# Optimization experiments

Measured on AMD Instinct MI355X. Metric: run time of the kernel, lower is better.

## Reference

```python
import jax, jax.numpy as jnp
import numpy as np

N, F_IN, F_OUT = 8192, 512, 256


def setup_inputs() -> dict:
    key = jax.random.key(0)
    k1, k2, k3, k4 = jax.random.split(key, 4)
    x = jax.random.normal(k1, (N, F_IN), dtype=jnp.float32)
    adj = jax.random.randint(k2, (N, N), 0, 2, dtype=jnp.int32)
    # xavier-uniform-like init scale for W and a
    wb = 1.414 * np.sqrt(6.0 / (F_IN + F_OUT))
    ab = 1.414 * np.sqrt(6.0 / (2 * F_OUT + 1))
    W = jax.random.uniform(k3, (F_IN, F_OUT), minval=-wb, maxval=wb, dtype=jnp.float32)
    a = jax.random.uniform(k4, (2 * F_OUT, 1), minval=-ab, maxval=ab, dtype=jnp.float32)
    return {"x": x, "adj": adj, "W": W, "a": a, "heads": 4}


def reference(x, adj, W, a, heads):
    # Wh = x @ W : [N, F_OUT]
    Wh = x @ W
    f_out = W.shape[1]
    # a = [a_src; a_dst], so e_ij = leakyrelu(Wh_i . a_src + Wh_j . a_dst)
    s_src = Wh @ a[:f_out, 0]   # [N]
    s_dst = Wh @ a[f_out:, 0]   # [N]
    e = jax.nn.leaky_relu(s_src[:, None] + s_dst[None, :], negative_slope=0.2)  # [N, N]
    # scatter into dense matrix: non-edges hold 0 and DO participate in softmax
    att = jnp.where(adj != 0, e, jnp.zeros((), dtype=e.dtype))
    att = jax.nn.softmax(att, axis=1)
    # dropout is identity in eval mode (self.training=False)
    h = att @ Wh                                  # [N, F_OUT]
    n = x.shape[0]
    h = h.reshape(n, heads, f_out // heads).mean(axis=1)  # multi-head mean
    return h
```

## Files before the change

### kernel.cpp

```cpp
#include <hip/hip_runtime.h>
#include <hip/hip_bf16.h>

#define NN 8192
#define FIN 512
#define FOUT 256
#define FH 64
#define JSPLIT 32
#define JCHUNK (NN / JSPLIT)
#define STEPS (JCHUNK / 32)

typedef float f32x16 __attribute__((ext_vector_type(16)));
typedef short bf16x8 __attribute__((ext_vector_type(8)));
typedef unsigned short us8 __attribute__((ext_vector_type(8)));
typedef unsigned int uint32x4 __attribute__((ext_vector_type(4)));

static __device__ __forceinline__ unsigned short f2bf(float x) {
  unsigned int u = __builtin_bit_cast(unsigned int, x);
  unsigned int r = (u + 0x7fffu + ((u >> 16) & 1u)) >> 16;
  return (unsigned short)r;
}
static __device__ __forceinline__ float bf2f(unsigned short u) {
  unsigned int v = ((unsigned int)u) << 16;
  return __builtin_bit_cast(float, v);
}
static __device__ __forceinline__ float fastexp2(float x) {
  float r;
  asm("v_exp_f32 %0, %1" : "=v"(r) : "v"(x));
  return r;
}
static __device__ __forceinline__ unsigned int pkbf(float a, float b) {
  unsigned int w;
  asm("v_cvt_pk_bf16_f32 %0, %1, %2" : "=v"(w) : "v"(a), "v"(b));
  return w;
}
static __device__ __forceinline__ float lo16f(unsigned int w) {
  return __builtin_bit_cast(float, w << 16);
}
static __device__ __forceinline__ float hi16f(unsigned int w) {
  return __builtin_bit_cast(float, w & 0xffff0000u);
}

__global__ __launch_bounds__(256) void prep_small(const float* __restrict__ W,
                                                  const float* __restrict__ a,
                                                  unsigned short* __restrict__ Bw) {
  const int kt = blockIdx.x;
  __shared__ float wm[16][64];
  __shared__ float wt[16][2];
  const int t = threadIdx.x;
#pragma unroll
  for (int i = 0; i < 4; ++i) {
    const int idx = t + i * 256;
    const int kr = idx >> 6, c = idx & 63;
    const float* wr = W + (size_t)(kt * 16 + kr) * FOUT + c;
    wm[kr][c] = 0.25f * (wr[0] + wr[64] + wr[128] + wr[192]);
  }
  if (t < 32) {
    const int kr = t & 15, sel = t >> 4;
    const float* wr = W + (size_t)(kt * 16 + kr) * FOUT;
    const float* av = a + sel * FOUT;
    float s = 0.f;
    for (int n = 0; n < FOUT; ++n) s += wr[n] * av[n];
    wt[kr][sel] = s * 1.44269504f;
  }
  __syncthreads();
#pragma unroll
  for (int i = 0; i < 12; ++i) {
    const int idx = t + i * 256;
    const int e = idx & 7, n = (idx >> 3) & 31, r2 = idx >> 8;
    const int khb = r2 & 1, q = r2 >> 1;
    const int nf = q % 3, h = q / 3;
    const int k = khb * 8 + e;
    float v = nf < 2 ? wm[k][nf * 32 + n]
                     : (n == 0 ? wt[k][0] : (n == 1 ? wt[k][1] : 0.f));
    const unsigned short hi = f2bf(v);
    Bw[(size_t)kt * 3072 + idx] = (h == 0) ? hi : f2bf(v - bf2f(hi));
  }
}

__global__ __launch_bounds__(192) void gemm_whm(const float* __restrict__ X,
                                                const unsigned short* __restrict__ Bw,
                                                unsigned short* __restrict__ Bg,
                                                float* __restrict__ ssrc,
                                                float* __restrict__ sdst) {
  __shared__ float xs[32][516];
  __shared__ float sred[32][2];
  const int mw = blockIdx.x;
  const int tid = threadIdx.x;
  const float* xb = X + (size_t)(mw * 32) * FIN;
  for (int i = tid; i < 4096; i += 192) {
    const int row = i >> 7, c4 = (i & 127) << 2;
    *(float4*)&xs[row][c4] = *(const float4*)(xb + (size_t)row * FIN + c4);
  }
  __syncthreads();

  const int nf = tid >> 6, lane = tid & 63;
  const int l31 = lane & 31, kh = lane >> 5;
  f32x16 acc = (f32x16)(0.f);
  const unsigned short* bp = Bw + ((size_t)nf * 2 + kh) * 256 + l31 * 8;
#pragma unroll 4
  for (int kt = 0; kt < 32; ++kt) {
    const float* xr = &xs[l31][kt * 16 + kh * 8];
    const float4 va = *(const float4*)xr;
    const float4 vb = *(const float4*)(xr + 4);
    const unsigned int h0 = pkbf(va.x, va.y), h1 = pkbf(va.z, va.w);
    const unsigned int h2 = pkbf(vb.x, vb.y), h3 = pkbf(vb.z, vb.w);
    const unsigned int l0 = pkbf(va.x - lo16f(h0), va.y - hi16f(h0));
    const unsigned int l1 = pkbf(va.z - lo16f(h1), va.w - hi16f(h1));
    const unsigned int l2 = pkbf(vb.x - lo16f(h2), vb.y - hi16f(h2));
    const unsigned int l3 = pkbf(vb.z - lo16f(h3), vb.w - hi16f(h3));
    const uint32x4 uh = {h0, h1, h2, h3}, ul = {l0, l1, l2, l3};
    const bf16x8 a_h = __builtin_bit_cast(bf16x8, uh);
    const bf16x8 a_l = __builtin_bit_cast(bf16x8, ul);
    const bf16x8 b_h = *(const bf16x8*)(bp + kt * 3072);
    const bf16x8 b_l = *(const bf16x8*)(bp + kt * 3072 + 1536);
    acc = __builtin_amdgcn_mfma_f32_32x32x16_bf16(a_h, b_h, acc, 0, 0, 0);
    acc = __builtin_amdgcn_mfma_f32_32x32x16_bf16(a_h, b_l, acc, 0, 0, 0);
    acc = __builtin_amdgcn_mfma_f32_32x32x16_bf16(a_l, b_h, acc, 0, 0, 0);
  }
  if (nf < 2) {
    unsigned short* bgw = Bg + (size_t)mw * 2048;
#pragma unroll
    for (int reg = 0; reg < 16; reg += 2) {
      const unsigned int wh = pkbf(acc[reg], acc[reg + 1]);
      const int e = (reg & 3) | (kh << 2);
      const int khb = (reg >> 2) & 1;
      const int kc = reg >> 3;
      *(unsigned int*)(bgw + (size_t)(((kc * 2 + khb) * 2 + nf) * 256) +
                       l31 * 8 + e) = wh;
    }
  } else if (l31 < 2) {
#pragma unroll
    for (int reg = 0; reg < 16; ++reg) {
      const int row = (reg & 3) + ((reg >> 2) << 3) + (kh << 2);
      sred[row][l31] = acc[reg];
    }
  }
  __syncthreads();
  if (threadIdx.x < 32) {
    ssrc[mw * 32 + threadIdx.x] = sred[threadIdx.x][0];
    sdst[mw * 32 + threadIdx.x] = sred[threadIdx.x][1];
  }
}

#define GLL(G, L)                                                           \
  __builtin_amdgcn_global_load_lds(                                         \
      (const __attribute__((address_space(1))) unsigned int*)(G),           \
      (__attribute__((address_space(3))) unsigned int*)(L), 16, 0, 0)

#define PEL(P, MM, B, SD)                    \
  float P;                                   \
  {                                          \
    float tt = ss + (SD);                    \
    float lr = fmaxf(tt, 0.2f * tt);         \
    lr = (((MM) >> (B)) & 1u) ? lr : 0.0f;   \
    P = fastexp2(lr);                        \
    dacc += P;                               \
  }

#define GENAF(AF, M0, M1, M2, M3, KC4, SA, SB)                            \
  {                                                                       \
    PEL(p0, M0, (KC4) + 0, (SA).x) PEL(p1, M1, (KC4) + 0, (SA).y)         \
    PEL(p2, M2, (KC4) + 0, (SA).z) PEL(p3, M3, (KC4) + 0, (SA).w)         \
    PEL(p4, M0, (KC4) + 1, (SB).x) PEL(p5, M1, (KC4) + 1, (SB).y)         \
    PEL(p6, M2, (KC4) + 1, (SB).z) PEL(p7, M3, (KC4) + 1, (SB).w)         \
    const uint32x4 uv = {pkbf(p0, p1), pkbf(p2, p3), pkbf(p4, p5),        \
                         pkbf(p6, p7)};                                   \
    AF = __builtin_bit_cast(bf16x8, uv);                                  \
  }

__global__ __launch_bounds__(512, 4) void gat_aggr(
    const int* __restrict__ adj, const float* __restrict__ ssrc_g,
    const float* __restrict__ sdst_g, const unsigned short* __restrict__ Bg,
    unsigned short* __restrict__ Upb, float* __restrict__ Dp) {
  __shared__ unsigned short lbuf[STEPS * 2048];
  __shared__ float sds[256];
  const int bid = blockIdx.x;
  const int bj = bid & 31, bm = bid >> 5;
  const int wv = threadIdx.x >> 6, lane = threadIdx.x & 63;
  const int l31 = lane & 31, kh = lane >> 5;
  const int rbase = bm * 256;
  const int myrow = rbase + wv * 32 + l31;
  const int jb = bj * JCHUNK;
  const float ss = ssrc_g[myrow];

  {
    const unsigned short* gs = Bg + (size_t)bj * (STEPS * 2048) +
                               (size_t)(wv * 4) * 512 + lane * 8;
#pragma unroll
    for (int c = 0; c < 4; ++c) GLL(gs + c * 512, &lbuf[(wv * 4 + c) * 512]);
    if (wv == 0) GLL(sdst_g + jb + lane * 4, &sds[0]);
  }

  unsigned long long mb0 = 0, mb1 = 0, mb2 = 0, mb3 = 0;
  {
    const int* abase = adj + (size_t)(rbase + wv * 32) * NN + jb + lane * 4;
#pragma unroll 1
    for (int rd = 0; rd < 4; ++rd) {
      int4 q0 = *(const int4*)(abase + (size_t)(rd * 8 + 0) * NN);
      int4 q1 = *(const int4*)(abase + (size_t)(rd * 8 + 1) * NN);
      int4 q2 = *(const int4*)(abase + (size_t)(rd * 8 + 2) * NN);
      int4 q3 = *(const int4*)(abase + (size_t)(rd * 8 + 3) * NN);
      int4 q4 = *(const int4*)(abase + (size_t)(rd * 8 + 4) * NN);
      int4 q5 = *(const int4*)(abase + (size_t)(rd * 8 + 5) * NN);
      int4 q6 = *(const int4*)(abase + (size_t)(rd * 8 + 6) * NN);
      int4 q7 = *(const int4*)(abase + (size_t)(rd * 8 + 7) * NN);
#define BAL(Q, I)                                                   \
      {                                                             \
        unsigned long long b0 = __ballot((Q).x != 0);               \
        unsigned long long b1 = __ballot((Q).y != 0);               \
        unsigned long long b2 = __ballot((Q).z != 0);               \
        unsigned long long b3 = __ballot((Q).w != 0);               \
        const bool keep = (l31 == rd * 8 + (I));                    \
        mb0 = keep ? b0 : mb0;                                      \
        mb1 = keep ? b1 : mb1;                                      \
        mb2 = keep ? b2 : mb2;                                      \
        mb3 = keep ? b3 : mb3;                                      \
      }
      BAL(q0, 0) BAL(q1, 1) BAL(q2, 2) BAL(q3, 3)
      BAL(q4, 4) BAL(q5, 5) BAL(q6, 6) BAL(q7, 7)
#undef BAL
    }
  }

  f32x16 acc0 = (f32x16)(0.f), acc1 = (f32x16)(0.f);
  float dacc = 0.f;
  __syncthreads();

  const unsigned short* lb0 = &lbuf[kh * 512 + l31 * 8];
  const float* sdl = &sds[kh * 8];
  const int kh2 = kh * 2;

#pragma unroll 1
  for (int t = 0; t < STEPS; ++t) {
    const unsigned int m0 = ((unsigned int)mb0) >> kh2;
    const unsigned int m1 = ((unsigned int)mb1) >> kh2;
    const unsigned int m2 = ((unsigned int)mb2) >> kh2;
    const unsigned int m3 = ((unsigned int)mb3) >> kh2;
    mb0 >>= 8; mb1 >>= 8; mb2 >>= 8; mb3 >>= 8;
    const unsigned short* tb = lb0 + (size_t)t * 2048;
    const bf16x8 b00 = *(const bf16x8*)(tb);
    const bf16x8 b01 = *(const bf16x8*)(tb + 256);
    const bf16x8 b10 = *(const bf16x8*)(tb + 1024);
    const bf16x8 b11 = *(const bf16x8*)(tb + 1280);
    const float4 sA0 = *(const float4*)(sdl + t * 32);
    const float4 sB0 = *(const float4*)(sdl + t * 32 + 4);
    const float4 sA1 = *(const float4*)(sdl + t * 32 + 16);
    const float4 sB1 = *(const float4*)(sdl + t * 32 + 20);
    bf16x8 af0, af1;
    GENAF(af0, m0, m1, m2, m3, 0, sA0, sB0)
    GENAF(af1, m0, m1, m2, m3, 4, sA1, sB1)
    acc0 = __builtin_amdgcn_mfma_f32_32x32x16_bf16(af0, b00, acc0, 0, 0, 0);
    acc1 = __builtin_amdgcn_mfma_f32_32x32x16_bf16(af0, b01, acc1, 0, 0, 0);
    acc0 = __builtin_amdgcn_mfma_f32_32x32x16_bf16(af1, b10, acc0, 0, 0, 0);
    acc1 = __builtin_amdgcn_mfma_f32_32x32x16_bf16(af1, b11, acc1, 0, 0, 0);
  }

  dacc += __shfl_xor(dacc, 32);
  if (lane < 32) Dp[(size_t)bj * NN + myrow] = dacc;

  unsigned short* ub = Upb + ((size_t)bj * NN + rbase + wv * 32) * FH;
#pragma unroll
  for (int reg = 0; reg < 16; ++reg) {
    const int rr = (reg & 3) + ((reg >> 2) << 3) + (kh << 2);
    ub[(size_t)rr * FH + l31] = f2bf(acc0[reg]);
    ub[(size_t)rr * FH + 32 + l31] = f2bf(acc1[reg]);
  }
}

__global__ __launch_bounds__(256) void finalize(const unsigned short* __restrict__ Upb,
                                                const float* __restrict__ Dp,
                                                float* __restrict__ out) {
  const int idx = blockIdx.x * 256 + threadIdx.x;
  const int i = idx >> 6;
  float u = 0.f, d = 0.f;
#pragma unroll
  for (int s = 0; s < JSPLIT; ++s) {
    d += Dp[(size_t)s * NN + i];
    u += bf2f(Upb[(size_t)s * NN * FH + idx]);
  }
  out[idx] = u / d;
}

extern "C" void kernel_launch(void* const* d_in, const int* in_sizes, int n_in,
                              void* d_out, int out_size, void* d_ws, size_t ws_size,
                              hipStream_t stream) {
  const float* x = (const float*)d_in[0];
  const int* adj = (const int*)d_in[1];
  const float* W = (const float*)d_in[2];
  const float* a = (const float*)d_in[3];
  char* ws = (char*)d_ws;

  unsigned short* Upb = (unsigned short*)ws;
  unsigned short* Bg = (unsigned short*)(ws + ((size_t)32 << 20));
  unsigned short* Bw = (unsigned short*)(ws + ((size_t)36 << 20));
  float* ssrc = (float*)(ws + ((size_t)36 << 20) + (256u << 10));
  float* sdst = (float*)(ws + ((size_t)36 << 20) + (288u << 10));
  float* Dp = (float*)(ws + ((size_t)36 << 20) + (320u << 10));
  float* out = (float*)d_out;

  prep_small<<<32, 256, 0, stream>>>(W, a, Bw);
  gemm_whm<<<256, 192, 0, stream>>>(x, Bw, Bg, ssrc, sdst);
  gat_aggr<<<32 * JSPLIT, 512, 0, stream>>>(adj, ssrc, sdst, Bg, Upb, Dp);
  finalize<<<NN * FH / 256, 256, 0, stream>>>(Upb, Dp, out);
}
```

Before: 91.46 us.

## Stream adjacency chunks into the MFMA loop with register prefetch

Replaces the up-front load of all adjacency rows into 64-bit ballot masks with a chunked scheme. Each chunk covers 64 columns across 32 rows (16 lanes per row), is converted to 16-bit masks by ballot and shift, and the next chunk's loads are issued before the MFMA work on the current one. The aim is to overlap adjacency global-memory latency with compute rather than stalling before the main loop. The cost is extra shift and select work per ballot and a fully unrolled loop that may raise register pressure.

```diff
diff --git a/kernel.cpp b/kernel.cpp
--- a/kernel.cpp
+++ b/kernel.cpp
@@ -191,36 +191,16 @@
     if (wv == 0) GLL(sdst_g + jb + lane * 4, &sds[0]);
   }
 
-  unsigned long long mb0 = 0, mb1 = 0, mb2 = 0, mb3 = 0;
-  {
-    const int* abase = adj + (size_t)(rbase + wv * 32) * NN + jb + lane * 4;
-#pragma unroll 1
-    for (int rd = 0; rd < 4; ++rd) {
-      int4 q0 = *(const int4*)(abase + (size_t)(rd * 8 + 0) * NN);
-      int4 q1 = *(const int4*)(abase + (size_t)(rd * 8 + 1) * NN);
-      int4 q2 = *(const int4*)(abase + (size_t)(rd * 8 + 2) * NN);
-      int4 q3 = *(const int4*)(abase + (size_t)(rd * 8 + 3) * NN);
-      int4 q4 = *(const int4*)(abase + (size_t)(rd * 8 + 4) * NN);
-      int4 q5 = *(const int4*)(abase + (size_t)(rd * 8 + 5) * NN);
-      int4 q6 = *(const int4*)(abase + (size_t)(rd * 8 + 6) * NN);
-      int4 q7 = *(const int4*)(abase + (size_t)(rd * 8 + 7) * NN);
-#define BAL(Q, I)                                                   \
-      {                                                             \
-        unsigned long long b0 = __ballot((Q).x != 0);               \
-        unsigned long long b1 = __ballot((Q).y != 0);               \
-        unsigned long long b2 = __ballot((Q).z != 0);               \
-        unsigned long long b3 = __ballot((Q).w != 0);               \
-        const bool keep = (l31 == rd * 8 + (I));                    \
-        mb0 = keep ? b0 : mb0;                                      \
-        mb1 = keep ? b1 : mb1;                                      \
-        mb2 = keep ? b2 : mb2;                                      \
-        mb3 = keep ? b3 : mb3;                                      \
-      }
-      BAL(q0, 0) BAL(q1, 1) BAL(q2, 2) BAL(q3, 3)
-      BAL(q4, 4) BAL(q5, 5) BAL(q6, 6) BAL(q7, 7)
-#undef BAL
-    }
-  }
+  const int* achunk = adj + (size_t)(rbase + wv * 32 + (lane >> 4)) * NN + jb +
+                      (lane & 15) * 4;
+  int4 q0 = *(const int4*)(achunk + (size_t)0 * 4 * NN);
+  int4 q1 = *(const int4*)(achunk + (size_t)1 * 4 * NN);
+  int4 q2 = *(const int4*)(achunk + (size_t)2 * 4 * NN);
+  int4 q3 = *(const int4*)(achunk + (size_t)3 * 4 * NN);
+  int4 q4 = *(const int4*)(achunk + (size_t)4 * 4 * NN);
+  int4 q5 = *(const int4*)(achunk + (size_t)5 * 4 * NN);
+  int4 q6 = *(const int4*)(achunk + (size_t)6 * 4 * NN);
+  int4 q7 = *(const int4*)(achunk + (size_t)7 * 4 * NN);
 
   f32x16 acc0 = (f32x16)(0.f), acc1 = (f32x16)(0.f);
   float dacc = 0.f;
@@ -229,30 +209,65 @@
   const unsigned short* lb0 = &lbuf[kh * 512 + l31 * 8];
   const float* sdl = &sds[kh * 8];
   const int kh2 = kh * 2;
-
-#pragma unroll 1
-  for (int t = 0; t < STEPS; ++t) {
-    const unsigned int m0 = ((unsigned int)mb0) >> kh2;
-    const unsigned int m1 = ((unsigned int)mb1) >> kh2;
-    const unsigned int m2 = ((unsigned int)mb2) >> kh2;
-    const unsigned int m3 = ((unsigned int)mb3) >> kh2;
-    mb0 >>= 8; mb1 >>= 8; mb2 >>= 8; mb3 >>= 8;
-    const unsigned short* tb = lb0 + (size_t)t * 2048;
-    const bf16x8 b00 = *(const bf16x8*)(tb);
-    const bf16x8 b01 = *(const bf16x8*)(tb + 256);
-    const bf16x8 b10 = *(const bf16x8*)(tb + 1024);
-    const bf16x8 b11 = *(const bf16x8*)(tb + 1280);
-    const float4 sA0 = *(const float4*)(sdl + t * 32);
-    const float4 sB0 = *(const float4*)(sdl + t * 32 + 4);
-    const float4 sA1 = *(const float4*)(sdl + t * 32 + 16);
-    const float4 sB1 = *(const float4*)(sdl + t * 32 + 20);
-    bf16x8 af0, af1;
-    GENAF(af0, m0, m1, m2, m3, 0, sA0, sB0)
-    GENAF(af1, m0, m1, m2, m3, 4, sA1, sB1)
-    acc0 = __builtin_amdgcn_mfma_f32_32x32x16_bf16(af0, b00, acc0, 0, 0, 0);
-    acc1 = __builtin_amdgcn_mfma_f32_32x32x16_bf16(af0, b01, acc1, 0, 0, 0);
-    acc0 = __builtin_amdgcn_mfma_f32_32x32x16_bf16(af1, b10, acc0, 0, 0, 0);
-    acc1 = __builtin_amdgcn_mfma_f32_32x32x16_bf16(af1, b11, acc1, 0, 0, 0);
+  const int shx = (l31 & 3) * 16;
+
+#pragma unroll
+  for (int c = 0; c < 4; ++c) {
+    unsigned int mk0 = 0, mk1 = 0, mk2 = 0, mk3 = 0;
+#define BALX(Q, I)                                                  \
+    {                                                               \
+      const unsigned long long b0 = __ballot((Q).x != 0);           \
+      const unsigned long long b1 = __ballot((Q).y != 0);           \
+      const unsigned long long b2 = __ballot((Q).z != 0);           \
+      const unsigned long long b3 = __ballot((Q).w != 0);           \
+      const bool keep = ((l31 >> 2) == (I));                        \
+      const unsigned int e0 = (unsigned int)(b0 >> shx) & 0xffffu;  \
+      const unsigned int e1 = (unsigned int)(b1 >> shx) & 0xffffu;  \
+      const unsigned int e2 = (unsigned int)(b2 >> shx) & 0xffffu;  \
+      const unsigned int e3 = (unsigned int)(b3 >> shx) & 0xffffu;  \
+      mk0 = keep ? e0 : mk0;                                        \
+      mk1 = keep ? e1 : mk1;                                        \
+      mk2 = keep ? e2 : mk2;                                        \
+      mk3 = keep ? e3 : mk3;                                        \
+    }
+    BALX(q0, 0) BALX(q1, 1) BALX(q2, 2) BALX(q3, 3)
+    BALX(q4, 4) BALX(q5, 5) BALX(q6, 6) BALX(q7, 7)
+#undef BALX
+    if (c < 3) {
+      const int* an = achunk + (c + 1) * 64;
+      q0 = *(const int4*)(an + (size_t)0 * 4 * NN);
+      q1 = *(const int4*)(an + (size_t)1 * 4 * NN);
+      q2 = *(const int4*)(an + (size_t)2 * 4 * NN);
+      q3 = *(const int4*)(an + (size_t)3 * 4 * NN);
+      q4 = *(const int4*)(an + (size_t)4 * 4 * NN);
+      q5 = *(const int4*)(an + (size_t)5 * 4 * NN);
+      q6 = *(const int4*)(an + (size_t)6 * 4 * NN);
+      q7 = *(const int4*)(an + (size_t)7 * 4 * NN);
+    }
+#pragma unroll
+    for (int s = 0; s < 2; ++s) {
+      const int t = c * 2 + s;
+      const unsigned int m0 = mk0 >> (s * 8 + kh2);
+      const unsigned int m1 = mk1 >> (s * 8 + kh2);
+      const unsigned int m2 = mk2 >> (s * 8 + kh2);
+      const unsigned int m3 = mk3 >> (s * 8 + kh2);
+      const unsigned short* tb = lb0 + (size_t)t * 2048;
+      const bf16x8 b00 = *(const bf16x8*)(tb);
+      const bf16x8 b01 = *(const bf16x8*)(tb + 256);
+      const bf16x8 b10 = *(const bf16x8*)(tb + 1024);
+      const bf16x8 b11 = *(const bf16x8*)(tb + 1280);
+      const float4 sA0 = *(const float4*)(sdl + t * 32);
+      const float4 sB0 = *(const float4*)(sdl + t * 32 + 4);
+      const float4 sA1 = *(const float4*)(sdl + t * 32 + 16);
+      const float4 sB1 = *(const float4*)(sdl + t * 32 + 20);
+      bf16x8 af0, af1;
+      GENAF(af0, m0, m1, m2, m3, 0, sA0, sB0)
+      GENAF(af1, m0, m1, m2, m3, 4, sA1, sB1)
+      acc0 = __builtin_amdgcn_mfma_f32_32x32x16_bf16(af0, b00, acc0, 0, 0, 0);
+      acc1 = __builtin_amdgcn_mfma_f32_32x32x16_bf16(af0, b01, acc1, 0, 0, 0);
+      acc0 = __builtin_amdgcn_mfma_f32_32x32x16_bf16(af1, b10, acc0, 0, 0, 0);
+      acc1 = __builtin_amdgcn_mfma_f32_32x32x16_bf16(af1, b11, acc1, 0, 0, 0);
+    }
   }
 
   dacc += __shfl_xor(dacc, 32);
```

After: 101.9 us. 11.4% more time.

## Stream adjacency mask loads per step with double-buffered prefetch

Applied to the files above, without the earlier changes.

Replaces the upfront load and ballot of the whole 32x256 adjacency tile with per-step loads of 32x32 slabs. The slab for step t+2 is loaded while step t's MFMA work runs. Mask bits are rebuilt each step with four ballots per component and a lane-dependent select, so adjacency memory latency overlaps with compute instead of stalling before the loop. The cost is more ballots and select instructions per step, plus extra registers for the two in-flight slabs.

```diff
diff --git a/kernel.cpp b/kernel.cpp
--- a/kernel.cpp
+++ b/kernel.cpp
@@ -38,6 +38,14 @@
 }
 static __device__ __forceinline__ float hi16f(unsigned int w) {
   return __builtin_bit_cast(float, w & 0xffff0000u);
+}
+static __device__ __forceinline__ unsigned int ext4(int l31,
+    unsigned long long c0, unsigned long long c1,
+    unsigned long long c2, unsigned long long c3) {
+  unsigned long long s01 = (l31 & 8) ? c1 : c0;
+  unsigned long long s23 = (l31 & 8) ? c3 : c2;
+  unsigned long long s = (l31 & 16) ? s23 : s01;
+  return (unsigned int)(s >> ((l31 & 7) * 8)) & 0xffu;
 }
 
 __global__ __launch_bounds__(256) void prep_small(const float* __restrict__ W,
@@ -191,36 +199,16 @@
     if (wv == 0) GLL(sdst_g + jb + lane * 4, &sds[0]);
   }
 
-  unsigned long long mb0 = 0, mb1 = 0, mb2 = 0, mb3 = 0;
-  {
-    const int* abase = adj + (size_t)(rbase + wv * 32) * NN + jb + lane * 4;
-#pragma unroll 1
-    for (int rd = 0; rd < 4; ++rd) {
-      int4 q0 = *(const int4*)(abase + (size_t)(rd * 8 + 0) * NN);
-      int4 q1 = *(const int4*)(abase + (size_t)(rd * 8 + 1) * NN);
-      int4 q2 = *(const int4*)(abase + (size_t)(rd * 8 + 2) * NN);
-      int4 q3 = *(const int4*)(abase + (size_t)(rd * 8 + 3) * NN);
-      int4 q4 = *(const int4*)(abase + (size_t)(rd * 8 + 4) * NN);
-      int4 q5 = *(const int4*)(abase + (size_t)(rd * 8 + 5) * NN);
-      int4 q6 = *(const int4*)(abase + (size_t)(rd * 8 + 6) * NN);
-      int4 q7 = *(const int4*)(abase + (size_t)(rd * 8 + 7) * NN);
-#define BAL(Q, I)                                                   \
-      {                                                             \
-        unsigned long long b0 = __ballot((Q).x != 0);               \
-        unsigned long long b1 = __ballot((Q).y != 0);               \
-        unsigned long long b2 = __ballot((Q).z != 0);               \
-        unsigned long long b3 = __ballot((Q).w != 0);               \
-        const bool keep = (l31 == rd * 8 + (I));                    \
-        mb0 = keep ? b0 : mb0;                                      \
-        mb1 = keep ? b1 : mb1;                                      \
-        mb2 = keep ? b2 : mb2;                                      \
-        mb3 = keep ? b3 : mb3;                                      \
-      }
-      BAL(q0, 0) BAL(q1, 1) BAL(q2, 2) BAL(q3, 3)
-      BAL(q4, 4) BAL(q5, 5) BAL(q6, 6) BAL(q7, 7)
-#undef BAL
-    }
-  }
+  const int* astep = adj + (size_t)(rbase + wv * 32 + (lane >> 3)) * NN + jb +
+                     (lane & 7) * 4;
+  int4 qa0 = *(const int4*)(astep + (size_t)0 * 8 * NN);
+  int4 qa1 = *(const int4*)(astep + (size_t)1 * 8 * NN);
+  int4 qa2 = *(const int4*)(astep + (size_t)2 * 8 * NN);
+  int4 qa3 = *(const int4*)(astep + (size_t)3 * 8 * NN);
+  int4 qb0 = *(const int4*)(astep + (size_t)0 * 8 * NN + 32);
+  int4 qb1 = *(const int4*)(astep + (size_t)1 * 8 * NN + 32);
+  int4 qb2 = *(const int4*)(astep + (size_t)2 * 8 * NN + 32);
+  int4 qb3 = *(const int4*)(astep + (size_t)3 * 8 * NN + 32);
 
   f32x16 acc0 = (f32x16)(0.f), acc1 = (f32x16)(0.f);
   float dacc = 0.f;
@@ -230,30 +218,52 @@
   const float* sdl = &sds[kh * 8];
   const int kh2 = kh * 2;
 
+#define PSTEP(T, QS0, QS1, QS2, QS3, RELOAD)                                  \
+  {                                                                          \
+    const unsigned int mk0 = ext4(l31, __ballot((QS0).x != 0),               \
+        __ballot((QS1).x != 0), __ballot((QS2).x != 0), __ballot((QS3).x != 0)); \
+    const unsigned int mk1 = ext4(l31, __ballot((QS0).y != 0),               \
+        __ballot((QS1).y != 0), __ballot((QS2).y != 0), __ballot((QS3).y != 0)); \
+    const unsigned int mk2 = ext4(l31, __ballot((QS0).z != 0),               \
+        __ballot((QS1).z != 0), __ballot((QS2).z != 0), __ballot((QS3).z != 0)); \
+    const unsigned int mk3 = ext4(l31, __ballot((QS0).w != 0),               \
+        __ballot((QS1).w != 0), __ballot((QS2).w != 0), __ballot((QS3).w != 0)); \
+    if (RELOAD) {                                                            \
+      const int* an = astep + ((T) + 2) * 32;                                \
+      QS0 = *(const int4*)(an + (size_t)0 * 8 * NN);                         \
+      QS1 = *(const int4*)(an + (size_t)1 * 8 * NN);                         \
+      QS2 = *(const int4*)(an + (size_t)2 * 8 * NN);                         \
+      QS3 = *(const int4*)(an + (size_t)3 * 8 * NN);                         \
+    }                                                                        \
+    const unsigned int m0 = mk0 >> kh2, m1 = mk1 >> kh2;                     \
+    const unsigned int m2 = mk2 >> kh2, m3 = mk3 >> kh2;                     \
+    const unsigned short* tb = lb0 + (size_t)(T) * 2048;                     \
+    const bf16x8 b00 = *(const bf16x8*)(tb);                    \
+    const bf16x8 b01 = *(const bf16x8*)(tb + 256);              \
+    const bf16x8 b10 = *(const bf16x8*)(tb + 1024);             \
+    const bf16x8 b11 = *(const bf16x8*)(tb + 1280);             \
+    const float4 sA0 = *(const float4*)(sdl + (T) * 32);                     \
+    const float4 sB0 = *(const float4*)(sdl + (T) * 32 + 4);                 \
+    const float4 sA1 = *(const float4*)(sdl + (T) * 32 + 16);                \
+    const float4 sB1 = *(const float4*)(sdl + (T) * 32 + 20);                \
+    bf16x8 af0, af1;                                                         \
+    GENAF(af0, m0, m1, m2, m3, 0, sA0, sB0)                                  \
+    GENAF(af1, m0, m1, m2, m3, 4, sA1, sB1)                                  \
+    acc0 = __builtin_amdgcn_mfma_f32_32x32x16_bf16(af0, b00, acc0, 0, 0, 0); \
+    acc1 = __builtin_amdgcn_mfma_f32_32x32x16_bf16(af0, b01, acc1, 0, 0, 0); \
+    acc0 = __builtin_amdgcn_mfma_f32_32x32x16_bf16(af1, b10, acc0, 0, 0, 0); \
+    acc1 = __builtin_amdgcn_mfma_f32_32x32x16_bf16(af1, b11, acc1, 0, 0, 0); \
+  }
+
 #pragma unroll 1
-  for (int t = 0; t < STEPS; ++t) {
-    const unsigned int m0 = ((unsigned int)mb0) >> kh2;
-    const unsigned int m1 = ((unsigned int)mb1) >> kh2;
-    const unsigned int m2 = ((unsigned int)mb2) >> kh2;
-    const unsigned int m3 = ((unsigned int)mb3) >> kh2;
-    mb0 >>= 8; mb1 >>= 8; mb2 >>= 8; mb3 >>= 8;
-    const unsigned short* tb = lb0 + (size_t)t * 2048;
-    const bf16x8 b00 = *(const bf16x8*)(tb);
-    const bf16x8 b01 = *(const bf16x8*)(tb + 256);
-    const bf16x8 b10 = *(const bf16x8*)(tb + 1024);
-    const bf16x8 b11 = *(const bf16x8*)(tb + 1280);
-    const float4 sA0 = *(const float4*)(sdl + t * 32);
-    const float4 sB0 = *(const float4*)(sdl + t * 32 + 4);
-    const float4 sA1 = *(const float4*)(sdl + t * 32 + 16);
-    const float4 sB1 = *(const float4*)(sdl + t * 32 + 20);
-    bf16x8 af0, af1;
-    GENAF(af0, m0, m1, m2, m3, 0, sA0, sB0)
-    GENAF(af1, m0, m1, m2, m3, 4, sA1, sB1)
-    acc0 = __builtin_amdgcn_mfma_f32_32x32x16_bf16(af0, b00, acc0, 0, 0, 0);
-    acc1 = __builtin_amdgcn_mfma_f32_32x32x16_bf16(af0, b01, acc1, 0, 0, 0);
-    acc0 = __builtin_amdgcn_mfma_f32_32x32x16_bf16(af1, b10, acc0, 0, 0, 0);
-    acc1 = __builtin_amdgcn_mfma_f32_32x32x16_bf16(af1, b11, acc1, 0, 0, 0);
-  }
+  for (int it = 0; it < 3; ++it) {
+    const int t0 = 2 * it;
+    PSTEP(t0, qa0, qa1, qa2, qa3, 1)
+    PSTEP(t0 + 1, qb0, qb1, qb2, qb3, 1)
+  }
+  PSTEP(6, qa0, qa1, qa2, qa3, 0)
+  PSTEP(7, qb0, qb1, qb2, qb3, 0)
+#undef PSTEP
 
   dacc += __shfl_xor(dacc, 32);
   if (lane < 32) Dp[(size_t)bj * NN + myrow] = dacc;
```

Result: no change. 91.05 us (-0.4%).
